# Optimization experiments

Measured on AMD Instinct MI355X. Metric: run time of the kernel, lower is better.

Reference implementation:

```python
import jax, jax.numpy as jnp
import numpy as np

N = 32; AUD = 128; MO = 256; LXM = 128; L = 600; B = 20; BL = 30
AH = 256; AE = 256; HID = 1024; OUT = 256; DEPTH = 2
IN_DIM = MO + AE + LXM      # 640
GRU_IN = IN_DIM + HID       # 1664


def gelu(x):
    return jax.nn.gelu(x, approximate=False)


def conv1d(x, w, b, stride=1, pad=0):
    y = jax.lax.conv_general_dilated(x, w, (stride,), [(pad, pad)],
                                     dimension_numbers=('NCH', 'OIH', 'NCH'))
    return y + b[None, :, None]


def layernorm(x, g, b, eps=1e-5):
    mu = jnp.mean(x, -1, keepdims=True)
    var = jnp.mean((x - mu) ** 2, -1, keepdims=True)
    return (x - mu) * jax.lax.rsqrt(var + eps) * g + b


def gru_cell(x, h, wih, whh, bih, bhh):
    gi = x @ wih.T + bih
    gh = h @ whh.T + bhh
    ir, iz, inn = jnp.split(gi, 3, -1)
    hr, hz, hn = jnp.split(gh, 3, -1)
    r = jax.nn.sigmoid(ir + hr)
    z = jax.nn.sigmoid(iz + hz)
    n = jnp.tanh(inn + r * hn)
    return (1.0 - z) * n + z * h


def setup_inputs():
    key = jax.random.key(0)
    ks = jax.random.split(key, 32)
    rn = lambda i, sh: jax.random.normal(ks[i], sh, jnp.float32) * 0.02
    z = lambda d: jnp.zeros((d,), jnp.float32)
    return {
        'aud': jax.random.normal(ks[0], (N, AUD, L), jnp.float32),
        'mo': jax.random.normal(ks[1], (N, MO, L), jnp.float32),
        'lxm': jax.random.normal(ks[2], (N, LXM, B), jnp.float32),
        'ae_w0': rn(3, (AH, AUD, 7)), 'ae_b0': z(AH),
        'ae_w1': rn(4, (AH, AH, 5)), 'ae_b1': z(AH),
        'ae_w2': rn(5, (AE, AH, 4)), 'ae_b2': z(AE),
        'ae_w3': rn(6, (AE, AE)), 'ae_b3': z(AE),
        'ae_ln_g': jnp.ones((AE,), jnp.float32), 'ae_ln_b': z(AE),
        'ci_w0': rn(7, (HID, MO + LXM)), 'ci_b0': z(HID),
        'ci_w1': rn(8, (HID, HID)), 'ci_b1': z(HID),
        'ci_w2': rn(9, (HID * DEPTH, HID)), 'ci_b2': z(HID * DEPTH),
        'dec_in_w': rn(10, (HID, IN_DIM)), 'dec_in_b': z(HID),
        'gru_wih0': rn(11, (3 * HID, GRU_IN)), 'gru_whh0': rn(12, (3 * HID, HID)),
        'gru_bih0': z(3 * HID), 'gru_bhh0': z(3 * HID),
        'gru_wih1': rn(13, (3 * HID, HID)), 'gru_whh1': rn(14, (3 * HID, HID)),
        'gru_bih1': z(3 * HID), 'gru_bhh1': z(3 * HID),
        'dec_ln_g': jnp.ones((HID,), jnp.float32), 'dec_ln_b': z(HID),
        'pred_w': rn(15, (OUT, HID)), 'pred_b': z(OUT),
    }


def reference(aud, mo, lxm, ae_w0, ae_b0, ae_w1, ae_b1, ae_w2, ae_b2, ae_w3, ae_b3,
              ae_ln_g, ae_ln_b, ci_w0, ci_b0, ci_w1, ci_b1, ci_w2, ci_b2,
              dec_in_w, dec_in_b, gru_wih0, gru_whh0, gru_bih0, gru_bhh0,
              gru_wih1, gru_whh1, gru_bih1, gru_bhh1, dec_ln_g, dec_ln_b,
              pred_w, pred_b):
    Nb = B - 2
    # Overlapping 3*BL audio windows for all blocks, encoded in one batched pass.
    win = jnp.stack([aud[:, :, b * BL:(b + 3) * BL] for b in range(Nb)], 0)  # [Nb,N,AUD,3BL]
    x = win.reshape(Nb * N, AUD, 3 * BL)
    x = gelu(conv1d(x, ae_w0, ae_b0))
    x = gelu(conv1d(x, ae_w1, ae_b1))
    x = gelu(conv1d(x, ae_w2, ae_b2, stride=2, pad=1))
    x = jnp.transpose(x, (0, 2, 1))                  # NDL -> NLD
    x = gelu(x @ ae_w3.T + ae_b3)
    x = layernorm(x, ae_ln_g, ae_ln_b)
    # Only frames 0..BL-1 of each encoded window are consumed by the decode loop.
    aud_seq = jnp.transpose(x[:, :BL, :].reshape(Nb, N, BL, AE), (0, 2, 1, 3)).reshape(Nb * BL, N, AE)
    lxm_seq = jnp.repeat(jnp.transpose(lxm[:, :, 1:B - 1], (2, 0, 1)), BL, axis=0)  # [T,N,LXM]
    # Cell state initializer.
    ci = gelu(jnp.concatenate([mo[:, :, BL - 1], lxm[:, :, 0]], -1) @ ci_w0.T + ci_b0)
    ci = gelu(ci @ ci_w1.T + ci_b1)
    h0 = jnp.transpose((ci @ ci_w2.T + ci_b2).reshape(N, DEPTH, HID), (1, 0, 2))  # [DEPTH,N,HID]

    def step(carry, inputs):
        pre_mo, h = carry
        a_t, l_t = inputs
        xcat = jnp.concatenate([pre_mo, a_t, l_t], -1)
        emb = gelu(xcat @ dec_in_w.T + dec_in_b)
        gin = jnp.concatenate([emb, xcat], -1)
        h0n = gru_cell(gin, h[0], gru_wih0, gru_whh0, gru_bih0, gru_bhh0)
        h1n = gru_cell(h0n, h[1], gru_wih1, gru_whh1, gru_bih1, gru_bhh1)
        pred = layernorm(h1n, dec_ln_g, dec_ln_b) @ pred_w.T + pred_b
        return (pred, jnp.stack([h0n, h1n])), pred

    _, preds = jax.lax.scan(step, (mo[:, :, BL - 1], h0), (aud_seq, lxm_seq))
    return jnp.transpose(preds, (1, 2, 0))  # [N, OUT, (B-2)*BL]
```

## Files before the change

### kernel.cpp

```cpp
#include <hip/hip_runtime.h>


typedef unsigned short u16;
typedef __attribute__((ext_vector_type(8))) short short8;
typedef __attribute__((ext_vector_type(4))) float f32x4;

#define GELU_FLG 1
#define BF16_FLG 2
#define NBLK 212
#define DEC_STEPS 540

__device__ __forceinline__ u16 f2b(float f){
  union { float f; unsigned u; } c; c.f = f;
  return (u16)((c.u + 0x7fffu + ((c.u >> 16) & 1u)) >> 16);
}
__device__ __forceinline__ short8 ld8(const u16* p){
  return *reinterpret_cast<const short8*>(p);
}
__device__ __forceinline__ short8 lds8(const void* p){
  return *reinterpret_cast<const short8*>(p);
}
__device__ __forceinline__ float ldfc(const float* p){
  return __hip_atomic_load(p, __ATOMIC_RELAXED, __HIP_MEMORY_SCOPE_AGENT);
}
__device__ __forceinline__ void stfc(float* p, float v){
  __hip_atomic_store(p, v, __ATOMIC_RELAXED, __HIP_MEMORY_SCOPE_AGENT);
}
__device__ __forceinline__ void stu32c(void* p, unsigned v){
  __hip_atomic_store((unsigned*)p, v, __ATOMIC_RELAXED, __HIP_MEMORY_SCOPE_AGENT);
}
__device__ __forceinline__ void st16c(u16* p, unsigned v){
  asm volatile("global_store_short %0, %1, off sc0 sc1" :: "v"(p), "v"(v) : "memory");
}
__device__ __forceinline__ f32x4 mfma16(short8 a, short8 b, f32x4 c){
  return __builtin_amdgcn_mfma_f32_16x16x32_bf16(a, b, c, 0, 0, 0);
}
__device__ __forceinline__ float gelu_f(float x){
  return 0.5f * x * (1.f + erff(x * 0.70710678118654752f));
}
__device__ __forceinline__ float sigmoid_f(float x){
  return 1.f / (1.f + __expf(-x));
}
__device__ __forceinline__ float tanh_f(float x){
  float e = __expf(-2.f * x);
  return (1.f - e) / (1.f + e);
}

template<int KB>
__device__ __forceinline__ void stageN(unsigned* ldsbase, const void* gbase, int lane, int q){
  const char* g = (const char*)gbase;
  #pragma unroll
  for (int c = 0; c < KB / 4; ++c){
    int cc = q + c * 4;
    __builtin_amdgcn_global_load_lds((const unsigned*)(g + (size_t)cc * 1024 + lane * 16),
                                     ldsbase + cc * 256, 16, 0, 0);
  }
}


__global__ void f2b_k(const float* __restrict__ s, u16* __restrict__ d, int n){
  int i = blockIdx.x * 256 + threadIdx.x;
  if (i < n) d[i] = f2b(s[i]);
}

__global__ void gather_xc_k(const float* __restrict__ mo, const float* __restrict__ lxm,
                            u16* __restrict__ xc, u16* __restrict__ pre_mo){
  int i = blockIdx.x * 256 + threadIdx.x;
  if (i >= 32 * 384) return;
  int n = i / 384, c = i - n * 384;
  float v = (c < 256) ? mo[(size_t)(n * 256 + c) * 600 + 29]
                      : lxm[(size_t)(n * 128 + (c - 256)) * 20];
  u16 h = f2b(v);
  xc[i] = h;
  if (c < 256) pre_mo[n * 256 + c] = h;
}

__global__ void lxm_g_k(const float* __restrict__ lxm, u16* __restrict__ o){
  int i = blockIdx.x * 256 + threadIdx.x;
  if (i >= 18 * 32 * 128) return;
  int c = i & 127, rest = i >> 7;
  int n = rest & 31, b = rest >> 5;
  o[i] = f2b(lxm[(size_t)(n * 128 + c) * 20 + 1 + b]);
}

__global__ void split_h_k(const float* __restrict__ hraw, u16* __restrict__ h0, u16* __restrict__ h1,
                          float* __restrict__ h0f, float* __restrict__ h1f){
  int i = blockIdx.x * 256 + threadIdx.x;
  if (i >= 32 * 1024) return;
  int n = i >> 10, c = i & 1023;
  float a = hraw[(size_t)n * 2048 + c];
  float b = hraw[(size_t)n * 2048 + 1024 + c];
  h0[i] = f2b(a); h1[i] = f2b(b);
  h0f[i] = a;     h1f[i] = b;
}

__global__ void build_xc0_k(const u16* __restrict__ pre_mo, const u16* __restrict__ aud_seq,
                            const u16* __restrict__ lxm_b, u16* __restrict__ xc0){
  int i = blockIdx.x * 256 + threadIdx.x;
  if (i >= 32 * 640) return;
  int n = i / 640, c = i - n * 640;
  u16 v;
  if (c < 256) v = pre_mo[n * 256 + c];
  else if (c < 512) v = aud_seq[n * 256 + (c - 256)];
  else v = lxm_b[n * 128 + (c - 512)];
  xc0[i] = v;
}

__global__ void swz_emb_k(const u16* __restrict__ src, u16* __restrict__ dst){
  int i = blockIdx.x * 256 + threadIdx.x;
  if (i >= 32 * 1024) return;
  int row = i >> 10, col = i & 1023;
  unsigned boff = (unsigned)(row * 2048) + (((unsigned)col * 2) ^ ((row & 7) << 4));
  *(u16*)((char*)dst + boff) = src[i];
}

__global__ void t_wpT_k(const float* __restrict__ wp, u16* __restrict__ wpT){
  int i = blockIdx.x * 256 + threadIdx.x;
  if (i >= 1024 * 256) return;
  int h = i >> 8, j = i & 255;
  wpT[i] = f2b(wp[(size_t)j * 1024 + h]);
}

__global__ void foldW_k(const float* __restrict__ src, const float* __restrict__ g,
                        const float* __restrict__ b, const float* __restrict__ addb,
                        u16* __restrict__ Wg, float* __restrict__ S, float* __restrict__ B, int R){
  int row = blockIdx.x * 4 + (threadIdx.x >> 6);
  if (row >= R) return;
  int lane = threadIdx.x & 63;
  const float* sr = src + (size_t)row * 1024;
  float s = 0.f, bb = 0.f;
  #pragma unroll
  for (int k = 0; k < 16; ++k){
    int c = lane + k * 64;
    float w = sr[c], gw = w * g[c];
    Wg[(size_t)row * 1024 + c] = f2b(gw);
    s += gw; bb += w * b[c];
  }
  #pragma unroll
  for (int m = 1; m < 64; m <<= 1){ s += __shfl_xor(s, m); bb += __shfl_xor(bb, m); }
  if (lane == 0){ S[row] = s; B[row] = bb + (addb ? addb[row] : 0.f); }
}

__global__ void vfold_k(const float* __restrict__ W, int ldw, int off, const float* __restrict__ pb,
                        const float* __restrict__ base, float* __restrict__ v, int R){
  int row = blockIdx.x * 4 + (threadIdx.x >> 6);
  if (row >= R) return;
  int lane = threadIdx.x & 63;
  const float* wr = W + (size_t)row * ldw + off;
  float s = 0.f;
  #pragma unroll
  for (int k = 0; k < 4; ++k){ int j = lane + k * 64; s += wr[j] * pb[j]; }
  #pragma unroll
  for (int m = 1; m < 64; m <<= 1) s += __shfl_xor(s, m);
  if (lane == 0) v[row] = s + (base ? base[row] : 0.f);
}


__global__ void im2col0_k(const float* __restrict__ aud, u16* __restrict__ A, int row0, long long tot){
  long long i = (long long)blockIdx.x * 256 + threadIdx.x;
  if (i >= tot) return;
  int k = (int)(i % 896);
  int row = row0 + (int)(i / 896);
  int ci = k / 7, kk = k - ci * 7;
  int p = row % 84, bn = row / 84;
  int b = bn >> 5, n = bn & 31;
  A[i] = f2b(aud[(size_t)(n * 128 + ci) * 600 + b * 30 + p + kk]);
}

__global__ void im2col1_k(const u16* __restrict__ O0, u16* __restrict__ A, int row0, long long tot){
  long long i = (long long)blockIdx.x * 256 + threadIdx.x;
  if (i >= tot) return;
  int k = (int)(i % 1280);
  int row = row0 + (int)(i / 1280);
  int ci = k / 5, kk = k - ci * 5;
  int p = row % 80, bn = row / 80;
  A[i] = O0[(size_t)(bn * 84 + p + kk) * 256 + ci];
}

__global__ void im2col2_k(const u16* __restrict__ O1, u16* __restrict__ A, int row0, long long tot){
  long long i = (long long)blockIdx.x * 256 + threadIdx.x;
  if (i >= tot) return;
  int k = (int)(i & 1023);
  int row = row0 + (int)(i >> 10);
  int ci = k >> 2, kk = k & 3;
  int p = row % 40, bn = row / 40;
  int pos = 2 * p - 1 + kk;
  A[i] = (pos >= 0 && pos < 80) ? O1[(size_t)(bn * 80 + pos) * 256 + ci] : (u16)0;
}


__global__ void gemm_bt(const u16* __restrict__ A, int lda,
                        const u16* __restrict__ W, int ldw, const float* __restrict__ bias,
                        void* __restrict__ outp, int M, int N, int K, int flags){
  const int lane = threadIdx.x & 63, widx = threadIdx.x >> 6;
  const int m0 = blockIdx.x * 64 + widx * 16;
  if (m0 >= M) return;
  const int n0 = blockIdx.y * 64;
  const int r = lane & 15, g4 = lane >> 4;
  const u16* arow = A + (size_t)(m0 + r) * lda + g4 * 8;
  const u16* wrow = W + (size_t)(n0 + r) * ldw + g4 * 8;
  f32x4 acc[4];
  const f32x4 FZ = {0.f, 0.f, 0.f, 0.f};
  acc[0] = FZ; acc[1] = FZ; acc[2] = FZ; acc[3] = FZ;
  for (int k = 0; k < K; k += 32){
    short8 a = ld8(arow + k);
    #pragma unroll
    for (int j = 0; j < 4; ++j)
      acc[j] = mfma16(a, ld8(wrow + (size_t)j * 16 * ldw + k), acc[j]);
  }
  #pragma unroll
  for (int j = 0; j < 4; ++j){
    int col = n0 + j * 16 + r;
    float bv = bias ? bias[col] : 0.f;
    #pragma unroll
    for (int q = 0; q < 4; ++q){
      int row = m0 + g4 * 4 + q;
      float v = acc[j][q] + bv;
      if (flags & GELU_FLG) v = gelu_f(v);
      if (flags & BF16_FLG) ((u16*)outp)[(size_t)row * N + col] = f2b(v);
      else                  ((float*)outp)[(size_t)row * N + col] = v;
    }
  }
}


__global__ void enc_ln_k(const float* __restrict__ O3, const float* __restrict__ g,
                         const float* __restrict__ bb, u16* __restrict__ aud_seq){
  int rid = blockIdx.x * 4 + (threadIdx.x >> 6);
  int lane = threadIdx.x & 63;
  int b = rid / 960, rem = rid - b * 960;
  int p2 = rem >> 5, n = rem & 31;
  int orow = (b * 32 + n) * 40 + p2;
  const float4 v = *reinterpret_cast<const float4*>(O3 + (size_t)orow * 256 + lane * 4);
  float s  = v.x + v.y + v.z + v.w;
  float s2 = v.x * v.x + v.y * v.y + v.z * v.z + v.w * v.w;
  #pragma unroll
  for (int m = 1; m < 64; m <<= 1){ s += __shfl_xor(s, m); s2 += __shfl_xor(s2, m); }
  float mu = s * (1.f / 256.f);
  float var = s2 * (1.f / 256.f) - mu * mu;
  float rs = rsqrtf(var + 1e-5f);
  int c = lane * 4;
  u16* dst = aud_seq + (size_t)rid * 256 + c;
  dst[0] = f2b((v.x - mu) * rs * g[c + 0] + bb[c + 0]);
  dst[1] = f2b((v.y - mu) * rs * g[c + 1] + bb[c + 1]);
  dst[2] = f2b((v.z - mu) * rs * g[c + 2] + bb[c + 2]);
  dst[3] = f2b((v.w - mu) * rs * g[c + 3] + bb[c + 3]);
}


struct DecArgs {
  const u16 *aud_seq, *lxm_b;
  const u16 *wih0, *whh0, *wih1, *whh1, *wd;
  const u16 *wpg, *Wdpg, *Wgpg;
  const float *Sp, *Bp, *S1, *B1, *S2, *B2, *vX, *vG;
  const float *bih0, *bhh0, *bih1, *bhh1;
  const u16 *h0init, *h1init;
  u16 *embR, *h0R, *h1R;
  float *statsR;
  float *GxR, *XalR, *GalR;
  float *h0f, *h1f, *out;
  int *sync;
};

__device__ __forceinline__ void sigslot(int* slot, int ep){
  asm volatile("s_waitcnt vmcnt(0)" ::: "memory");
  __syncthreads();
  if (threadIdx.x == 0)
    __hip_atomic_store(slot, ep, __ATOMIC_RELAXED, __HIP_MEMORY_SCOPE_AGENT);
}
__device__ __forceinline__ void wait_grp(const int* slotG, int nx, const int* slotE, int tgt){
  if (threadIdx.x < 64){
    const int lane = threadIdx.x;
    for (;;){
      int v = __hip_atomic_load(slotG + lane * 16, __ATOMIC_RELAXED, __HIP_MEMORY_SCOPE_AGENT);
      bool ok = (v >= tgt);
      if (lane < nx){
        int v2 = __hip_atomic_load(slotE + lane * 16, __ATOMIC_RELAXED, __HIP_MEMORY_SCOPE_AGENT);
        ok = ok && (v2 >= tgt);
      }
      if (__all(ok)) break;
      __builtin_amdgcn_s_sleep(1);
    }
  }
  __syncthreads();
}
__device__ __forceinline__ void stage_fence(){
  asm volatile("s_waitcnt vmcnt(0)" ::: "memory");
  __syncthreads();
}

__global__ __launch_bounds__(256, 1) void decode_k(DecArgs A){
  const int tid = threadIdx.x;
  const int lane = tid & 63, q = tid >> 6;
  const int r = lane & 15, g4 = lane >> 4;
  const int blk = blockIdx.x;
  __shared__ __align__(16) unsigned smw[25088];
  char* const stg = (char*)smw;
  float* const exch = (float*)(smw + 16384);
  float* const stgStats = (float*)(smw + 16384);
  const f32x4 FZ = {0.f, 0.f, 0.f, 0.f};
  const int sw = (r & 7) << 4;
  int* const slotH0 = A.sync;
  int* const slotH1 = A.sync + 128 * 16;
  int* const slotPE = A.sync + 256 * 16;
  int* const slotAL = A.sync + 384 * 16;

  if (blk < 64){
    const int c0 = blk * 16;
    const int kq = q * 256;
    int* const mySlot = slotH0 + blk * 16;
    short8 we[24], wh[24];
    #pragma unroll
    for (int g = 0; g < 3; ++g)
      #pragma unroll
      for (int ch = 0; ch < 8; ++ch){
        we[g * 8 + ch] = ld8(A.wih0 + (size_t)(g * 1024 + c0 + r) * 1664 + kq + ch * 32 + g4 * 8);
        wh[g * 8 + ch] = ld8(A.whh0 + (size_t)(g * 1024 + c0 + r) * 1024 + kq + ch * 32 + g4 * 8);
      }
    const int n_c = tid >> 3;
    const int cc0 = (tid & 7) * 2;
    const int colA = c0 + cc0, colB = colA + 1;
    const unsigned stoff = (unsigned)(n_c * 2048) + (((unsigned)colA * 2) ^ ((n_c & 7) << 4));
    const float bi_r[2] = {A.bih0[colA], A.bih0[colB]};
    const float bi_z[2] = {A.bih0[1024 + colA], A.bih0[1024 + colB]};
    const float bi_n[2] = {A.bih0[2048 + colA], A.bih0[2048 + colB]};
    const float bh_r[2] = {A.bhh0[colA], A.bhh0[colB]};
    const float bh_z[2] = {A.bhh0[1024 + colA], A.bhh0[1024 + colB]};
    const float bh_n[2] = {A.bhh0[2048 + colA], A.bhh0[2048 + colB]};
    f32x4 ar[2], az[2], ani[2], anh[2];
    ar[0] = FZ; ar[1] = FZ; az[0] = FZ; az[1] = FZ; ani[0] = FZ; ani[1] = FZ; anh[0] = FZ; anh[1] = FZ;
    #pragma unroll
    for (int ch = 0; ch < 8; ++ch){
      short8 a0 = ld8(A.h0init + r * 1024 + kq + ch * 32 + g4 * 8);
      short8 a1 = ld8(A.h0init + (16 + r) * 1024 + kq + ch * 32 + g4 * 8);
      ar[0] = mfma16(a0, wh[ch], ar[0]);        ar[1] = mfma16(a1, wh[ch], ar[1]);
      az[0] = mfma16(a0, wh[8 + ch], az[0]);    az[1] = mfma16(a1, wh[8 + ch], az[1]);
      anh[0] = mfma16(a0, wh[16 + ch], anh[0]); anh[1] = mfma16(a1, wh[16 + ch], anh[1]);
    }
    #pragma unroll 1
    for (int t = 0; t < DEC_STEPS; ++t){
      if (t > 0) wait_grp(slotPE, 4, slotPE + 64 * 16, t);
      const u16*  embT = A.embR + (size_t)t * 32768;
      u16*        h0T  = A.h0R  + (size_t)t * 32768;
      const float* GxT = A.GxR + (size_t)(t & 7) * 98304;
      stageN<64>(smw, embT, lane, q);
      float pgr[2], pgz[2], pgn[2], phf[2];
      #pragma unroll
      for (int e = 0; e < 2; ++e){
        int col = c0 + cc0 + e;
        pgr[e] = ldfc(GxT + n_c * 3072 + col);
        pgz[e] = ldfc(GxT + n_c * 3072 + 1024 + col);
        pgn[e] = ldfc(GxT + n_c * 3072 + 2048 + col);
        phf[e] = A.h0f[n_c * 1024 + col];
      }
      stage_fence();
      #pragma unroll
      for (int ch = 0; ch < 8; ++ch){
        int off = ((kq + ch * 32 + g4 * 8) * 2) ^ sw;
        short8 a0 = lds8(stg + r * 2048 + off);
        short8 a1 = lds8(stg + (16 + r) * 2048 + off);
        ar[0] = mfma16(a0, we[ch], ar[0]);        ar[1] = mfma16(a1, we[ch], ar[1]);
        az[0] = mfma16(a0, we[8 + ch], az[0]);    az[1] = mfma16(a1, we[8 + ch], az[1]);
        ani[0] = mfma16(a0, we[16 + ch], ani[0]); ani[1] = mfma16(a1, we[16 + ch], ani[1]);
      }
      #pragma unroll
      for (int m = 0; m < 2; ++m)
        #pragma unroll
        for (int j = 0; j < 4; ++j){
          int row = m * 16 + g4 * 4 + j;
          exch[((q * 4 + 0) * 32 + row) * 17 + r] = ar[m][j];
          exch[((q * 4 + 1) * 32 + row) * 17 + r] = az[m][j];
          exch[((q * 4 + 2) * 32 + row) * 17 + r] = ani[m][j];
          exch[((q * 4 + 3) * 32 + row) * 17 + r] = anh[m][j];
        }
      __syncthreads();
      float hv2[2];
      #pragma unroll
      for (int e = 0; e < 2; ++e){
        int cc = cc0 + e, col = c0 + cc;
        float sr = bi_r[e] + bh_r[e] + pgr[e];
        float sz = bi_z[e] + bh_z[e] + pgz[e];
        float si = bi_n[e] + pgn[e];
        float sh = bh_n[e];
        #pragma unroll
        for (int qq = 0; qq < 4; ++qq){
          sr += exch[((qq * 4 + 0) * 32 + n_c) * 17 + cc];
          sz += exch[((qq * 4 + 1) * 32 + n_c) * 17 + cc];
          si += exch[((qq * 4 + 2) * 32 + n_c) * 17 + cc];
          sh += exch[((qq * 4 + 3) * 32 + n_c) * 17 + cc];
        }
        float rg = sigmoid_f(sr), zg = sigmoid_f(sz);
        float ng = tanh_f(si + rg * sh);
        float hv = (1.f - zg) * ng + zg * phf[e];
        A.h0f[n_c * 1024 + col] = hv;
        hv2[e] = hv;
      }
      stu32c((char*)h0T + stoff,
             (unsigned)f2b(hv2[0]) | ((unsigned)f2b(hv2[1]) << 16));
      __syncthreads();
      sigslot(mySlot, t + 1);
      wait_grp(slotH0, 0, slotH0, t + 1);
      stageN<64>(smw, h0T, lane, q);
      stage_fence();
      ar[0] = FZ; ar[1] = FZ; az[0] = FZ; az[1] = FZ; ani[0] = FZ; ani[1] = FZ; anh[0] = FZ; anh[1] = FZ;
      #pragma unroll
      for (int ch = 0; ch < 8; ++ch){
        int off = ((kq + ch * 32 + g4 * 8) * 2) ^ sw;
        short8 a0 = lds8(stg + r * 2048 + off);
        short8 a1 = lds8(stg + (16 + r) * 2048 + off);
        ar[0] = mfma16(a0, wh[ch], ar[0]);        ar[1] = mfma16(a1, wh[ch], ar[1]);
        az[0] = mfma16(a0, wh[8 + ch], az[0]);    az[1] = mfma16(a1, wh[8 + ch], az[1]);
        anh[0] = mfma16(a0, wh[16 + ch], anh[0]); anh[1] = mfma16(a1, wh[16 + ch], anh[1]);
      }
    }
  } else if (blk < 128){
    const int c0 = (blk - 64) * 16;
    const int kq = q * 256;
    int* const mySlot = slotH1 + (blk - 64) * 16;
    short8 wi[24], wh[24];
    #pragma unroll
    for (int g = 0; g < 3; ++g)
      #pragma unroll
      for (int ch = 0; ch < 8; ++ch){
        wi[g * 8 + ch] = ld8(A.wih1 + (size_t)(g * 1024 + c0 + r) * 1024 + kq + ch * 32 + g4 * 8);
        wh[g * 8 + ch] = ld8(A.whh1 + (size_t)(g * 1024 + c0 + r) * 1024 + kq + ch * 32 + g4 * 8);
      }
    const int n_c = tid >> 3;
    const int cc0 = (tid & 7) * 2;
    const int colA = c0 + cc0, colB = colA + 1;
    const unsigned stoff = (unsigned)(n_c * 2048) + (((unsigned)colA * 2) ^ ((n_c & 7) << 4));
    const float bi_r[2] = {A.bih1[colA], A.bih1[colB]};
    const float bi_z[2] = {A.bih1[1024 + colA], A.bih1[1024 + colB]};
    const float bi_n[2] = {A.bih1[2048 + colA], A.bih1[2048 + colB]};
    const float bh_r[2] = {A.bhh1[colA], A.bhh1[colB]};
    const float bh_z[2] = {A.bhh1[1024 + colA], A.bhh1[1024 + colB]};
    const float bh_n[2] = {A.bhh1[2048 + colA], A.bhh1[2048 + colB]};
    f32x4 ar[2], az[2], ani[2], anh[2];
    ar[0] = FZ; ar[1] = FZ; az[0] = FZ; az[1] = FZ; ani[0] = FZ; ani[1] = FZ; anh[0] = FZ; anh[1] = FZ;
    #pragma unroll
    for (int ch = 0; ch < 8; ++ch){
      short8 a0 = ld8(A.h1init + r * 1024 + kq + ch * 32 + g4 * 8);
      short8 a1 = ld8(A.h1init + (16 + r) * 1024 + kq + ch * 32 + g4 * 8);
      ar[0] = mfma16(a0, wh[ch], ar[0]);        ar[1] = mfma16(a1, wh[ch], ar[1]);
      az[0] = mfma16(a0, wh[8 + ch], az[0]);    az[1] = mfma16(a1, wh[8 + ch], az[1]);
      anh[0] = mfma16(a0, wh[16 + ch], anh[0]); anh[1] = mfma16(a1, wh[16 + ch], anh[1]);
    }
    #pragma unroll 1
    for (int t = 0; t < DEC_STEPS; ++t){
      wait_grp(slotH0, 0, slotH0, t + 1);
      const u16* h0T = A.h0R + (size_t)t * 32768;
      u16*       h1T = A.h1R + (size_t)t * 32768;
      stageN<64>(smw, h0T, lane, q);
      float phf[2];
      phf[0] = A.h1f[n_c * 1024 + colA];
      phf[1] = A.h1f[n_c * 1024 + colB];
      stage_fence();
      #pragma unroll
      for (int ch = 0; ch < 8; ++ch){
        int off = ((kq + ch * 32 + g4 * 8) * 2) ^ sw;
        short8 a0 = lds8(stg + r * 2048 + off);
        short8 a1 = lds8(stg + (16 + r) * 2048 + off);
        ar[0] = mfma16(a0, wi[ch], ar[0]);        ar[1] = mfma16(a1, wi[ch], ar[1]);
        az[0] = mfma16(a0, wi[8 + ch], az[0]);    az[1] = mfma16(a1, wi[8 + ch], az[1]);
        ani[0] = mfma16(a0, wi[16 + ch], ani[0]); ani[1] = mfma16(a1, wi[16 + ch], ani[1]);
      }
      #pragma unroll
      for (int m = 0; m < 2; ++m)
        #pragma unroll
        for (int j = 0; j < 4; ++j){
          int row = m * 16 + g4 * 4 + j;
          exch[((q * 4 + 0) * 32 + row) * 17 + r] = ar[m][j];
          exch[((q * 4 + 1) * 32 + row) * 17 + r] = az[m][j];
          exch[((q * 4 + 2) * 32 + row) * 17 + r] = ani[m][j];
          exch[((q * 4 + 3) * 32 + row) * 17 + r] = anh[m][j];
        }
      __syncthreads();
      float hv2[2];
      #pragma unroll
      for (int e = 0; e < 2; ++e){
        int cc = cc0 + e, col = c0 + cc;
        float sr = bi_r[e] + bh_r[e];
        float sz = bi_z[e] + bh_z[e];
        float si = bi_n[e];
        float sh = bh_n[e];
        #pragma unroll
        for (int qq = 0; qq < 4; ++qq){
          sr += exch[((qq * 4 + 0) * 32 + n_c) * 17 + cc];
          sz += exch[((qq * 4 + 1) * 32 + n_c) * 17 + cc];
          si += exch[((qq * 4 + 2) * 32 + n_c) * 17 + cc];
          sh += exch[((qq * 4 + 3) * 32 + n_c) * 17 + cc];
        }
        float rg = sigmoid_f(sr), zg = sigmoid_f(sz);
        float ng = tanh_f(si + rg * sh);
        float hv = (1.f - zg) * ng + zg * phf[e];
        A.h1f[n_c * 1024 + col] = hv;
        hv2[e] = hv;
      }
      stu32c((char*)h1T + stoff,
             (unsigned)f2b(hv2[0]) | ((unsigned)f2b(hv2[1]) << 16));
      float sv = hv2[0] + hv2[1], sq = hv2[0] * hv2[0] + hv2[1] * hv2[1];
      sv += __shfl_xor(sv, 1); sq += __shfl_xor(sq, 1);
      sv += __shfl_xor(sv, 2); sq += __shfl_xor(sq, 2);
      sv += __shfl_xor(sv, 4); sq += __shfl_xor(sq, 4);
      if ((tid & 7) == 0){
        stfc(A.statsR + (size_t)t * 4096 + (blk - 64) * 64 + n_c, sv);
        stfc(A.statsR + (size_t)t * 4096 + (blk - 64) * 64 + 32 + n_c, sq);
      }
      __syncthreads();
      sigslot(mySlot, t + 1);
      wait_grp(slotH1, 0, slotH1, t + 1);
      stageN<64>(smw, h1T, lane, q);
      stage_fence();
      ar[0] = FZ; ar[1] = FZ; az[0] = FZ; az[1] = FZ; ani[0] = FZ; ani[1] = FZ; anh[0] = FZ; anh[1] = FZ;
      #pragma unroll
      for (int ch = 0; ch < 8; ++ch){
        int off = ((kq + ch * 32 + g4 * 8) * 2) ^ sw;
        short8 a0 = lds8(stg + r * 2048 + off);
        short8 a1 = lds8(stg + (16 + r) * 2048 + off);
        ar[0] = mfma16(a0, wh[ch], ar[0]);        ar[1] = mfma16(a1, wh[ch], ar[1]);
        az[0] = mfma16(a0, wh[8 + ch], az[0]);    az[1] = mfma16(a1, wh[8 + ch], az[1]);
        anh[0] = mfma16(a0, wh[16 + ch], anh[0]); anh[1] = mfma16(a1, wh[16 + ch], anh[1]);
      }
    }
  } else if (blk < 196){
    const int tile = (blk - 128) * 4 + q;
    int* const mySlot = slotPE + (blk - 128) * 16;
    int jt, c0;
    const u16* wsrc; const float *Sv, *Bv;
    if (tile < 16)      { jt = 0; c0 = tile * 16;        wsrc = A.wpg;  Sv = A.Sp; Bv = A.Bp; }
    else if (tile < 80) { jt = 1; c0 = (tile - 16) * 16; wsrc = A.Wdpg; Sv = A.S1; Bv = A.B1; }
    else                { jt = 2; c0 = (tile - 80) * 16; wsrc = A.Wgpg; Sv = A.S2; Bv = A.B2; }
    short8 w[32];
    #pragma unroll
    for (int ch = 0; ch < 32; ++ch)
      w[ch] = ld8(wsrc + (size_t)(c0 + r) * 1024 + ch * 32 + g4 * 8);
    const float Sc = Sv[c0 + r], Bc = Bv[c0 + r];
    const int col = c0 + r;
    #pragma unroll 1
    for (int t = 0; t < DEC_STEPS; ++t){
      wait_grp(slotH1, 16, slotAL, t + 1);
      const u16*   h1T = A.h1R + (size_t)t * 32768;
      const float* stT = A.statsR + (size_t)t * 4096;
      const int sl = (t + 1) & 7;
      stageN<64>(smw, h1T, lane, q);
      stageN<16>(smw + 16384, stT, lane, q);
      const float* XalT = A.XalR + (size_t)sl * 32768;
      const float* GalT = A.GalR + (size_t)sl * 98304;
      float addv[2][4];
      #pragma unroll
      for (int m = 0; m < 2; ++m)
        #pragma unroll
        for (int j = 0; j < 4; ++j){
          int n = m * 16 + g4 * 4 + j;
          addv[m][j] = (jt == 1) ? ldfc(XalT + n * 1024 + col)
                     : (jt == 2) ? ldfc(GalT + n * 3072 + col) : 0.f;
        }
      stage_fence();
      float sacc = 0.f;
      #pragma unroll
      for (int b2 = 0; b2 < 64; ++b2) sacc += stgStats[b2 * 64 + lane];
      float muA[2][4], rsA[2][4];
      #pragma unroll
      for (int m = 0; m < 2; ++m)
        #pragma unroll
        for (int j = 0; j < 4; ++j){
          int n = m * 16 + g4 * 4 + j;
          float sv = __shfl(sacc, n), sq = __shfl(sacc, 32 + n);
          float mu = sv * (1.f / 1024.f);
          muA[m][j] = mu;
          rsA[m][j] = rsqrtf(sq * (1.f / 1024.f) - mu * mu + 1e-5f);
        }
      f32x4 a0 = FZ, a1 = FZ;
      #pragma unroll
      for (int ch = 0; ch < 32; ++ch){
        int off = ((ch * 32 + g4 * 8) * 2) ^ sw;
        short8 x0 = lds8(stg + r * 2048 + off);
        short8 x1 = lds8(stg + (16 + r) * 2048 + off);
        a0 = mfma16(x0, w[ch], a0);
        a1 = mfma16(x1, w[ch], a1);
      }
      u16*   embN = A.embR + (size_t)(t + 1) * 32768;
      float* GxN  = A.GxR + (size_t)sl * 98304;
      #pragma unroll
      for (int m = 0; m < 2; ++m)
        #pragma unroll
        for (int j = 0; j < 4; ++j){
          int n = m * 16 + g4 * 4 + j;
          float acc = (m ? a1[j] : a0[j]);
          float v = rsA[m][j] * (acc - muA[m][j] * Sc) + Bc;
          if (jt == 0){
            A.out[(size_t)n * (256 * 540) + (size_t)col * 540 + t] = v;
          } else if (jt == 1){
            float pre = v + addv[m][j];
            unsigned boff = (unsigned)(n * 2048) + (((unsigned)col * 2) ^ ((n & 7) << 4));
            st16c((u16*)((char*)embN + boff), (unsigned)f2b(gelu_f(pre)));
          } else {
            stfc(GxN + n * 3072 + col, v + addv[m][j]);
          }
        }
      sigslot(mySlot, t + 1);
    }
  } else {
    const int wg = (blk - 196) * 4 + q;
    int* const mySlot = slotAL + (blk - 196) * 16;
    const int at0 = wg * 4;
    short8 w[48];
    float vb[4];
    #pragma unroll
    for (int j = 0; j < 4; ++j){
      int at = at0 + j;
      if (at < 64){
        #pragma unroll
        for (int ch = 0; ch < 12; ++ch)
          w[j * 12 + ch] = ld8(A.wd + (size_t)(at * 16 + r) * 640 + 256 + ch * 32 + g4 * 8);
        vb[j] = A.vX[at * 16 + r];
      } else {
        #pragma unroll
        for (int ch = 0; ch < 12; ++ch)
          w[j * 12 + ch] = ld8(A.wih0 + (size_t)((at - 64) * 16 + r) * 1664 + 1280 + ch * 32 + g4 * 8);
        vb[j] = A.vG[(at - 64) * 16 + r];
      }
    }
    #pragma unroll 1
    for (int t = 0; t < DEC_STEPS; ++t){
      if (t >= 8) wait_grp(slotPE, 4, slotPE + 64 * 16, t - 7);
      const int tn = t + 1;
      const int tread = (tn > 539) ? 539 : tn;
      const int bn = tread / 30;
      const int sl = tn & 7;
      float* XalW = A.XalR + (size_t)sl * 32768;
      float* GalW = A.GalR + (size_t)sl * 98304;
      short8 af0[12], af1[12];
      #pragma unroll
      for (int ch = 0; ch < 12; ++ch){
        int kk = ch * 32 + g4 * 8;
        if (ch < 8){
          af0[ch] = ld8(A.aud_seq + ((size_t)tread * 32 + r) * 256 + kk);
          af1[ch] = ld8(A.aud_seq + ((size_t)tread * 32 + 16 + r) * 256 + kk);
        } else {
          af0[ch] = ld8(A.lxm_b + ((size_t)bn * 32 + r) * 128 + kk - 256);
          af1[ch] = ld8(A.lxm_b + ((size_t)bn * 32 + 16 + r) * 128 + kk - 256);
        }
      }
      #pragma unroll
      for (int j = 0; j < 4; ++j){
        f32x4 c0a = FZ, c1a = FZ;
        #pragma unroll
        for (int ch = 0; ch < 12; ++ch){
          c0a = mfma16(af0[ch], w[j * 12 + ch], c0a);
          c1a = mfma16(af1[ch], w[j * 12 + ch], c1a);
        }
        int at = at0 + j;
        #pragma unroll
        for (int m = 0; m < 2; ++m)
          #pragma unroll
          for (int jj = 0; jj < 4; ++jj){
            int n = m * 16 + g4 * 4 + jj;
            float v = (m ? c1a[jj] : c0a[jj]) + vb[j];
            if (at < 64) stfc(XalW + n * 1024 + at * 16 + r, v);
            else         stfc(GalW + n * 3072 + (at - 64) * 16 + r, v);
          }
      }
      sigslot(mySlot, tn);
    }
  }
}


extern "C" void kernel_launch(void* const* d_in, const int* in_sizes, int n_in,
                              void* d_out, int out_size, void* d_ws, size_t ws_size,
                              hipStream_t stream) {
  enum { I_AUD=0, I_MO=1, I_LXM=2, I_AEW0=3, I_AEB0=4, I_AEW1=5, I_AEB1=6, I_AEW2=7, I_AEB2=8,
         I_AEW3=9, I_AEB3=10, I_AELNG=11, I_AELNB=12, I_CIW0=13, I_CIB0=14, I_CIW1=15, I_CIB1=16,
         I_CIW2=17, I_CIB2=18, I_DECW=19, I_DECB=20, I_WIH0=21, I_WHH0=22, I_BIH0=23, I_BHH0=24,
         I_WIH1=25, I_WHH1=26, I_BIH1=27, I_BHH1=28, I_LNG=29, I_LNB=30, I_PREDW=31, I_PREDB=32 };

  char* base = (char*)d_ws;
  size_t off = 0;
  auto alloc = [&](size_t bytes)->void*{
    void* p = base + off;
    off += (bytes + 255) & ~(size_t)255;
    return p;
  };

  u16* wd_b   = (u16*)alloc((size_t)1024*640*2);
  u16* wih0_b = (u16*)alloc((size_t)3072*1664*2);
  u16* whh0_b = (u16*)alloc((size_t)3072*1024*2);
  u16* wih1_b = (u16*)alloc((size_t)3072*1024*2);
  u16* whh1_b = (u16*)alloc((size_t)3072*1024*2);
  u16* wc0    = (u16*)alloc((size_t)1024*384*2);
  u16* wc1    = (u16*)alloc((size_t)1024*1024*2);
  u16* wc2    = (u16*)alloc((size_t)2048*1024*2);
  u16* w0k    = (u16*)alloc((size_t)256*896*2);
  u16* w1k    = (u16*)alloc((size_t)256*1280*2);
  u16* w2k    = (u16*)alloc((size_t)256*1024*2);
  u16* w3k    = (u16*)alloc((size_t)256*256*2);
  u16* wpT    = (u16*)alloc((size_t)1024*256*2);
  u16* wpg    = (u16*)alloc((size_t)256*1024*2);
  u16* Wdpg   = (u16*)alloc((size_t)1024*1024*2);
  u16* Wgpg   = (u16*)alloc((size_t)3072*1024*2);
  float* Sp = (float*)alloc(256*4);   float* Bp = (float*)alloc(256*4);
  float* S1 = (float*)alloc(1024*4);  float* B1 = (float*)alloc(1024*4);
  float* S2 = (float*)alloc(3072*4);  float* B2 = (float*)alloc(3072*4);
  float* vX = (float*)alloc(1024*4);  float* vG = (float*)alloc(3072*4);
  u16* aud_seq = (u16*)alloc((size_t)540*32*256*2);
  u16* lxm_b   = (u16*)alloc((size_t)18*32*128*2);
  u16* xc      = (u16*)alloc((size_t)32*384*2);
  u16* xc0     = (u16*)alloc((size_t)32*640*2);
  u16* ci1     = (u16*)alloc((size_t)32*1024*2);
  u16* ci2     = (u16*)alloc((size_t)32*1024*2);
  float* hraw  = (float*)alloc((size_t)32*2048*4);
  u16* h0i     = (u16*)alloc((size_t)32*1024*2);
  u16* h1i     = (u16*)alloc((size_t)32*1024*2);
  float* h0f   = (float*)alloc((size_t)32*1024*4);
  float* h1f   = (float*)alloc((size_t)32*1024*4);
  u16* pre_mo  = (u16*)alloc((size_t)32*256*2);
  u16* emb0    = (u16*)alloc((size_t)32*1024*2);
  float* GxR   = (float*)alloc((size_t)8*32*3072*4);
  float* XalR  = (float*)alloc((size_t)8*32*1024*4);
  float* GalR  = (float*)alloc((size_t)8*32*3072*4);
  int* syncb   = (int*)alloc((size_t)512*16*4);
  char* enc_base = base + off;
  u16* O0   = (u16*)alloc((size_t)48384*256*2);
  u16* O1   = (u16*)alloc((size_t)46080*256*2);
  u16* O2   = (u16*)alloc((size_t)23040*256*2);
  float* O3 = (float*)alloc((size_t)23040*256*4);
  u16* Abuf = (u16*)alloc((size_t)23040*1280*2);
  float* Wdp_f = (float*)Abuf;
  float* Wgp_f = (float*)((char*)Abuf + (size_t)1024*1024*4 + 256);
  u16* embR     = (u16*)enc_base;
  u16* h0R      = embR + (size_t)541*32768;
  u16* h1R      = h0R + (size_t)540*32768;
  float* statsR = (float*)(h1R + (size_t)540*32768);
  (void)ws_size; (void)in_sizes; (void)n_in; (void)out_size;

  const float* aud = (const float*)d_in[I_AUD];
  const float* mo  = (const float*)d_in[I_MO];
  const float* lxm = (const float*)d_in[I_LXM];
  float* out = (float*)d_out;

  auto cdiv = [](long long a, long long b)->int{ return (int)((a + b - 1) / b); };
  auto cvt = [&](int idx, u16* dst, int n){
    f2b_k<<<cdiv(n,256), 256, 0, stream>>>((const float*)d_in[idx], dst, n);
  };

  cvt(I_DECW, wd_b,   1024*640);
  cvt(I_WIH0, wih0_b, 3072*1664);
  cvt(I_WHH0, whh0_b, 3072*1024);
  cvt(I_WIH1, wih1_b, 3072*1024);
  cvt(I_WHH1, whh1_b, 3072*1024);
  cvt(I_CIW0, wc0,    1024*384);
  cvt(I_CIW1, wc1,    1024*1024);
  cvt(I_CIW2, wc2,    2048*1024);
  cvt(I_AEW0, w0k,    256*896);
  cvt(I_AEW1, w1k,    256*1280);
  cvt(I_AEW2, w2k,    256*1024);
  cvt(I_AEW3, w3k,    256*256);

  for (int c = 0; c < 2; ++c){
    int row0 = c * 24192;
    long long tot = (long long)24192 * 896;
    im2col0_k<<<cdiv(tot,256), 256, 0, stream>>>(aud, Abuf, row0, tot);
    gemm_bt<<<dim3(24192/64, 4), 256, 0, stream>>>(Abuf, 896, w0k, 896, (const float*)d_in[I_AEB0],
        O0 + (size_t)row0*256, 24192, 256, 896, GELU_FLG|BF16_FLG);
  }
  for (int c = 0; c < 2; ++c){
    int row0 = c * 23040;
    long long tot = (long long)23040 * 1280;
    im2col1_k<<<cdiv(tot,256), 256, 0, stream>>>(O0, Abuf, row0, tot);
    gemm_bt<<<dim3(23040/64, 4), 256, 0, stream>>>(Abuf, 1280, w1k, 1280, (const float*)d_in[I_AEB1],
        O1 + (size_t)row0*256, 23040, 256, 1280, GELU_FLG|BF16_FLG);
  }
  {
    long long tot = (long long)23040 * 1024;
    im2col2_k<<<cdiv(tot,256), 256, 0, stream>>>(O1, Abuf, 0, tot);
    gemm_bt<<<dim3(23040/64, 4), 256, 0, stream>>>(Abuf, 1024, w2k, 1024, (const float*)d_in[I_AEB2],
        O2, 23040, 256, 1024, GELU_FLG|BF16_FLG);
  }
  gemm_bt<<<dim3(23040/64, 4), 256, 0, stream>>>(O2, 256, w3k, 256, (const float*)d_in[I_AEB3],
      O3, 23040, 256, 256, GELU_FLG);
  enc_ln_k<<<4320, 256, 0, stream>>>(O3, (const float*)d_in[I_AELNG], (const float*)d_in[I_AELNB], aud_seq);

  lxm_g_k<<<cdiv(18*32*128,256), 256, 0, stream>>>(lxm, lxm_b);
  gather_xc_k<<<cdiv(32*384,256), 256, 0, stream>>>(mo, lxm, xc, pre_mo);
  gemm_bt<<<dim3(1,16), 256, 0, stream>>>(xc, 384, wc0, 384, (const float*)d_in[I_CIB0],
      ci1, 32, 1024, 384, GELU_FLG|BF16_FLG);
  gemm_bt<<<dim3(1,16), 256, 0, stream>>>(ci1, 1024, wc1, 1024, (const float*)d_in[I_CIB1],
      ci2, 32, 1024, 1024, GELU_FLG|BF16_FLG);
  gemm_bt<<<dim3(1,32), 256, 0, stream>>>(ci2, 1024, wc2, 1024, (const float*)d_in[I_CIB2],
      hraw, 32, 2048, 1024, 0);
  split_h_k<<<cdiv(32*1024,256), 256, 0, stream>>>(hraw, h0i, h1i, h0f, h1f);

  t_wpT_k<<<cdiv(1024*256,256), 256, 0, stream>>>((const float*)d_in[I_PREDW], wpT);
  gemm_bt<<<dim3(16,16), 256, 0, stream>>>(wd_b, 640, wpT, 256, nullptr, Wdp_f, 1024, 1024, 256, 0);
  gemm_bt<<<dim3(48,16), 256, 0, stream>>>(wih0_b + 1024, 1664, wpT, 256, nullptr, Wgp_f, 3072, 1024, 256, 0);
  foldW_k<<<cdiv(1024,4), 256, 0, stream>>>(Wdp_f, (const float*)d_in[I_LNG], (const float*)d_in[I_LNB],
      nullptr, Wdpg, S1, B1, 1024);
  foldW_k<<<cdiv(3072,4), 256, 0, stream>>>(Wgp_f, (const float*)d_in[I_LNG], (const float*)d_in[I_LNB],
      nullptr, Wgpg, S2, B2, 3072);
  foldW_k<<<cdiv(256,4), 256, 0, stream>>>((const float*)d_in[I_PREDW], (const float*)d_in[I_LNG],
      (const float*)d_in[I_LNB], (const float*)d_in[I_PREDB], wpg, Sp, Bp, 256);
  vfold_k<<<cdiv(1024,4), 256, 0, stream>>>((const float*)d_in[I_DECW], 640, 0,
      (const float*)d_in[I_PREDB], (const float*)d_in[I_DECB], vX, 1024);
  vfold_k<<<cdiv(3072,4), 256, 0, stream>>>((const float*)d_in[I_WIH0], 1664, 1024,
      (const float*)d_in[I_PREDB], nullptr, vG, 3072);

  build_xc0_k<<<cdiv(32*640,256), 256, 0, stream>>>(pre_mo, aud_seq, lxm_b, xc0);
  gemm_bt<<<dim3(1,16), 256, 0, stream>>>(xc0, 640, wd_b, 640, (const float*)d_in[I_DECB],
      emb0, 32, 1024, 640, GELU_FLG|BF16_FLG);
  swz_emb_k<<<cdiv(32*1024,256), 256, 0, stream>>>(emb0, embR);
  gemm_bt<<<dim3(1,48), 256, 0, stream>>>(xc0, 640, wih0_b + 1024, 1664, nullptr,
      GxR, 32, 3072, 640, 0);

  hipMemsetAsync(syncb, 0, (size_t)512*16*4, stream);

  DecArgs da;
  da.aud_seq = aud_seq; da.lxm_b = lxm_b;
  da.wih0 = wih0_b; da.whh0 = whh0_b; da.wih1 = wih1_b; da.whh1 = whh1_b; da.wd = wd_b;
  da.wpg = wpg; da.Wdpg = Wdpg; da.Wgpg = Wgpg;
  da.Sp = Sp; da.Bp = Bp; da.S1 = S1; da.B1 = B1; da.S2 = S2; da.B2 = B2; da.vX = vX; da.vG = vG;
  da.bih0 = (const float*)d_in[I_BIH0]; da.bhh0 = (const float*)d_in[I_BHH0];
  da.bih1 = (const float*)d_in[I_BIH1]; da.bhh1 = (const float*)d_in[I_BHH1];
  da.h0init = h0i; da.h1init = h1i;
  da.embR = embR; da.h0R = h0R; da.h1R = h1R; da.statsR = statsR;
  da.GxR = GxR; da.XalR = XalR; da.GalR = GalR;
  da.h0f = h0f; da.h1f = h1f;
  da.out = out; da.sync = syncb;
  decode_k<<<dim3(NBLK), dim3(256), 0, stream>>>(da);
}
```

Measured before the change: 8.078 ms.

## Merge weight conversions, vectorize LDS exchange, drop barriers, narrow wait groups

Merges the twelve separate fp32-to-bf16 weight conversion launches into one kernel that uses a cumulative segment table, cutting launch overhead. In the GRU layer blocks, the partial-sum exchange through LDS now writes f32x4 vectors in a new interleaved layout, and the trailing __syncthreads before signalling is removed. The per-step wait on the prediction-embedding group is also narrowed to a different subset of slots. Dropping the barrier and changing the wait set risks races if something still depended on them.

Result: no change. 8.138 ms (+0.7%).

```diff
diff --git a/kernel.cpp b/kernel.cpp
--- a/kernel.cpp
+++ b/kernel.cpp
@@ -58,9 +58,17 @@
 }
 
 
-__global__ void f2b_k(const float* __restrict__ s, u16* __restrict__ d, int n){
+#define NCVT 12
+struct CvtA { const float* s[NCVT]; u16* d[NCVT]; int cum[NCVT + 1]; };
+
+__global__ void cvtall_k(CvtA A){
   int i = blockIdx.x * 256 + threadIdx.x;
-  if (i < n) d[i] = f2b(s[i]);
+  if (i >= A.cum[NCVT]) return;
+  int seg = 0;
+  #pragma unroll
+  for (int k = 1; k < NCVT; ++k) seg += (i >= A.cum[k]);
+  int local = i - A.cum[seg];
+  A.d[seg][local] = f2b(A.s[seg][local]);
 }
 
 __global__ void gather_xc_k(const float* __restrict__ mo, const float* __restrict__ lxm,
@@ -289,6 +297,9 @@
   __syncthreads();
 }
 
+#define EXG 544
+#define EXQ 2176
+
 __global__ __launch_bounds__(256, 1) void decode_k(DecArgs A){
   const int tid = threadIdx.x;
   const int lane = tid & 63, q = tid >> 6;
@@ -319,6 +330,7 @@
       }
     const int n_c = tid >> 3;
     const int cc0 = (tid & 7) * 2;
+    const int mh = n_c >> 4, g4h = (n_c >> 2) & 3, jh = n_c & 3;
     const int colA = c0 + cc0, colB = colA + 1;
     const unsigned stoff = (unsigned)(n_c * 2048) + (((unsigned)colA * 2) ^ ((n_c & 7) << 4));
     const float bi_r[2] = {A.bih0[colA], A.bih0[colB]};
@@ -339,7 +351,7 @@
     }
     #pragma unroll 1
     for (int t = 0; t < DEC_STEPS; ++t){
-      if (t > 0) wait_grp(slotPE, 4, slotPE + 64 * 16, t);
+      if (t > 0) wait_grp(slotPE + 4 * 16, 0, slotPE, t);
       const u16*  embT = A.embR + (size_t)t * 32768;
       u16*        h0T  = A.h0R  + (size_t)t * 32768;
       const float* GxT = A.GxR + (size_t)(t & 7) * 98304;
@@ -364,15 +376,13 @@
         ani[0] = mfma16(a0, we[16 + ch], ani[0]); ani[1] = mfma16(a1, we[16 + ch], ani[1]);
       }
       #pragma unroll
-      for (int m = 0; m < 2; ++m)
-        #pragma unroll
-        for (int j = 0; j < 4; ++j){
-          int row = m * 16 + g4 * 4 + j;
-          exch[((q * 4 + 0) * 32 + row) * 17 + r] = ar[m][j];
-          exch[((q * 4 + 1) * 32 + row) * 17 + r] = az[m][j];
-          exch[((q * 4 + 2) * 32 + row) * 17 + r] = ani[m][j];
-          exch[((q * 4 + 3) * 32 + row) * 17 + r] = anh[m][j];
-        }
+      for (int m = 0; m < 2; ++m){
+        int base = (((q * 4) * 2 + m) * 4 + g4) * 17 + r;
+        *(f32x4*)(exch + (base) * 4)            = ar[m];
+        *(f32x4*)(exch + (base) * 4 + EXG)      = az[m];
+        *(f32x4*)(exch + (base) * 4 + 2 * EXG)  = ani[m];
+        *(f32x4*)(exch + (base) * 4 + 3 * EXG)  = anh[m];
+      }
       __syncthreads();
       float hv2[2];
       #pragma unroll
@@ -384,10 +394,8 @@
         float sh = bh_n[e];
         #pragma unroll
         for (int qq = 0; qq < 4; ++qq){
-          sr += exch[((qq * 4 + 0) * 32 + n_c) * 17 + cc];
-          sz += exch[((qq * 4 + 1) * 32 + n_c) * 17 + cc];
-          si += exch[((qq * 4 + 2) * 32 + n_c) * 17 + cc];
-          sh += exch[((qq * 4 + 3) * 32 + n_c) * 17 + cc];
+          const float* eb = exch + ((((qq * 4) * 2 + mh) * 4 + g4h) * 17 + cc) * 4 + jh;
+          sr += eb[0]; sz += eb[EXG]; si += eb[2 * EXG]; sh += eb[3 * EXG];
         }
         float rg = sigmoid_f(sr), zg = sigmoid_f(sz);
         float ng = tanh_f(si + rg * sh);
@@ -397,7 +405,6 @@
       }
       stu32c((char*)h0T + stoff,
              (unsigned)f2b(hv2[0]) | ((unsigned)f2b(hv2[1]) << 16));
-      __syncthreads();
       sigslot(mySlot, t + 1);
       wait_grp(slotH0, 0, slotH0, t + 1);
       stageN<64>(smw, h0T, lane, q);
@@ -427,6 +434,7 @@
       }
     const int n_c = tid >> 3;
     const int cc0 = (tid & 7) * 2;
+    const int mh = n_c >> 4, g4h = (n_c >> 2) & 3, jh = n_c & 3;
     const int colA = c0 + cc0, colB = colA + 1;
     const unsigned stoff = (unsigned)(n_c * 2048) + (((unsigned)colA * 2) ^ ((n_c & 7) << 4));
     const float bi_r[2] = {A.bih1[colA], A.bih1[colB]};
@@ -465,15 +473,13 @@
         ani[0] = mfma16(a0, wi[16 + ch], ani[0]); ani[1] = mfma16(a1, wi[16 + ch], ani[1]);
       }
       #pragma unroll
-      for (int m = 0; m < 2; ++m)
-        #pragma unroll
-        for (int j = 0; j < 4; ++j){
-          int row = m * 16 + g4 * 4 + j;
-          exch[((q * 4 + 0) * 32 + row) * 17 + r] = ar[m][j];
-          exch[((q * 4 + 1) * 32 + row) * 17 + r] = az[m][j];
-          exch[((q * 4 + 2) * 32 + row) * 17 + r] = ani[m][j];
-          exch[((q * 4 + 3) * 32 + row) * 17 + r] = anh[m][j];
-        }
+      for (int m = 0; m < 2; ++m){
+        int base = (((q * 4) * 2 + m) * 4 + g4) * 17 + r;
+        *(f32x4*)(exch + (base) * 4)            = ar[m];
+        *(f32x4*)(exch + (base) * 4 + EXG)      = az[m];
+        *(f32x4*)(exch + (base) * 4 + 2 * EXG)  = ani[m];
+        *(f32x4*)(exch + (base) * 4 + 3 * EXG)  = anh[m];
+      }
       __syncthreads();
       float hv2[2];
       #pragma unroll
@@ -485,10 +491,8 @@
         float sh = bh_n[e];
         #pragma unroll
         for (int qq = 0; qq < 4; ++qq){
-          sr += exch[((qq * 4 + 0) * 32 + n_c) * 17 + cc];
-          sz += exch[((qq * 4 + 1) * 32 + n_c) * 17 + cc];
-          si += exch[((qq * 4 + 2) * 32 + n_c) * 17 + cc];
-          sh += exch[((qq * 4 + 3) * 32 + n_c) * 17 + cc];
+          const float* eb = exch + ((((qq * 4) * 2 + mh) * 4 + g4h) * 17 + cc) * 4 + jh;
+          sr += eb[0]; sz += eb[EXG]; si += eb[2 * EXG]; sh += eb[3 * EXG];
         }
         float rg = sigmoid_f(sr), zg = sigmoid_f(sz);
         float ng = tanh_f(si + rg * sh);
@@ -506,7 +510,6 @@
         stfc(A.statsR + (size_t)t * 4096 + (blk - 64) * 64 + n_c, sv);
         stfc(A.statsR + (size_t)t * 4096 + (blk - 64) * 64 + 32 + n_c, sq);
       }
-      __syncthreads();
       sigslot(mySlot, t + 1);
       wait_grp(slotH1, 0, slotH1, t + 1);
       stageN<64>(smw, h1T, lane, q);
@@ -623,7 +626,7 @@
     }
     #pragma unroll 1
     for (int t = 0; t < DEC_STEPS; ++t){
-      if (t >= 8) wait_grp(slotPE, 4, slotPE + 64 * 16, t - 7);
+      if (t >= 8) wait_grp(slotPE + 4 * 16, 0, slotPE, t - 7);
       const int tn = t + 1;
       const int tread = (tn > 539) ? 539 : tn;
       const int bn = tread / 30;
@@ -740,22 +743,26 @@
   float* out = (float*)d_out;
 
   auto cdiv = [](long long a, long long b)->int{ return (int)((a + b - 1) / b); };
-  auto cvt = [&](int idx, u16* dst, int n){
-    f2b_k<<<cdiv(n,256), 256, 0, stream>>>((const float*)d_in[idx], dst, n);
-  };
-
-  cvt(I_DECW, wd_b,   1024*640);
-  cvt(I_WIH0, wih0_b, 3072*1664);
-  cvt(I_WHH0, whh0_b, 3072*1024);
-  cvt(I_WIH1, wih1_b, 3072*1024);
-  cvt(I_WHH1, whh1_b, 3072*1024);
-  cvt(I_CIW0, wc0,    1024*384);
-  cvt(I_CIW1, wc1,    1024*1024);
-  cvt(I_CIW2, wc2,    2048*1024);
-  cvt(I_AEW0, w0k,    256*896);
-  cvt(I_AEW1, w1k,    256*1280);
-  cvt(I_AEW2, w2k,    256*1024);
-  cvt(I_AEW3, w3k,    256*256);
+
+  {
+    CvtA ca;
+    const int srcIdx[NCVT] = {I_DECW, I_WIH0, I_WHH0, I_WIH1, I_WHH1, I_CIW0,
+                              I_CIW1, I_CIW2, I_AEW0, I_AEW1, I_AEW2, I_AEW3};
+    u16* dsts[NCVT] = {wd_b, wih0_b, whh0_b, wih1_b, whh1_b, wc0, wc1, wc2,
+                       w0k, w1k, w2k, w3k};
+    const int ns[NCVT] = {1024*640, 3072*1664, 3072*1024, 3072*1024, 3072*1024,
+                          1024*384, 1024*1024, 2048*1024, 256*896, 256*1280,
+                          256*1024, 256*256};
+    int c = 0;
+    for (int k = 0; k < NCVT; ++k){
+      ca.s[k] = (const float*)d_in[srcIdx[k]];
+      ca.d[k] = dsts[k];
+      ca.cum[k] = c;
+      c += ns[k];
+    }
+    ca.cum[NCVT] = c;
+    cvtall_k<<<cdiv(c, 256), 256, 0, stream>>>(ca);
+  }
 
   for (int c = 0; c < 2; ++c){
     int row0 = c * 24192;
```
